# Kernel tuning notes

Measured on AMD Instinct MI355X. Metric: run time of the kernel, lower is better.

## Reference

```python
import jax, jax.numpy as jnp
import numpy as np

B, L, K = 256, 2048, 8
INV_SQRT2 = 0.7071067811865476


def _scalar_mul(d1, d2):
    # (a + b*w + c*w^2 + d*w^3)*(a' + ...) in Z[omega], omega = e^{i pi/4}, w^4 = -1
    a1, b1, c1, e1 = d1[..., 0], d1[..., 1], d1[..., 2], d1[..., 3]
    a2, b2, c2, e2 = d2[..., 0], d2[..., 1], d2[..., 2], d2[..., 3]
    A = a1 * a2 + b1 * e2 - c1 * c2 + e1 * b2
    Bc = a1 * b2 + b1 * a2 + c1 * e2 + e1 * c2
    C = a1 * c2 + b1 * b2 + c1 * a2 - e1 * e2
    D = a1 * e2 - b1 * c2 - c1 * b2 + e1 * a2
    return jnp.stack([A, Bc, C, D], axis=-1).astype(d1.dtype)


def setup_inputs() -> dict:
    key = jax.random.key(0)
    k1, k2, k3, k4 = jax.random.split(key, 4)
    coeffs1 = jax.random.randint(k1, (B, L, K, 4), 0, 2).astype(jnp.float32)
    coeffs2 = jax.random.randint(k2, (B, L, K, 4), 0, 2).astype(jnp.float32)
    power1 = jax.random.randint(k3, (B, L, K), 0, 2, dtype=jnp.int32)
    power2 = jax.random.randint(k4, (B, L, K), 0, 2, dtype=jnp.int32)
    return {"coeffs1": coeffs1, "coeffs2": coeffs2, "power1": power1, "power2": power2}


def reference(coeffs1, coeffs2, power1, power2):
    # __mul__: elementwise ring multiply, powers add
    z = _scalar_mul(coeffs1, coeffs2)          # [B,L,K,4]
    zp = power1 + power2                        # [B,L,K]

    # reduce(): divide coeffs by 2 while all even (and nonzero), bump power
    def cond_fun(carry):
        c, _ = carry
        red = jnp.all(c % 2 == 0, axis=-1) & jnp.any(c != 0, axis=-1)
        return jnp.any(red)

    def body_fun(carry):
        c, p = carry
        red = jnp.all(c % 2 == 0, axis=-1) & jnp.any(c != 0, axis=-1)
        c = jnp.where(red[..., None], c // 2, c)
        p = jnp.where(red, p + 1, p)
        return (c, p)

    c, p = jax.lax.while_loop(cond_fun, body_fun, (z, zp))

    # prod(axis=2): associative scan of the ring multiply, take last; powers sum
    scanned = jax.lax.associative_scan(_scalar_mul, c, axis=2)
    pc = scanned[:, :, -1, :]                   # [B,L,4]
    pp = jnp.sum(p, axis=2)                     # [B,L]

    # sum(): align powers to the min over L (axis=-2 of coeffs), then sum
    minp = jnp.min(pp, axis=-1)                 # [B]
    align = (2.0 ** (pp - minp[..., None])).astype(pc.dtype)
    sc = jnp.sum(pc * align[..., None], axis=-2)  # [B,4]

    # to_complex(): c0 + c1*e^{i pi/4} + c2*i + c3*e^{-i pi/4}, scaled by 2^power
    real = sc[..., 0] + (sc[..., 1] + sc[..., 3]) * INV_SQRT2
    imag = sc[..., 2] + (sc[..., 1] - sc[..., 3]) * INV_SQRT2
    scale = (2.0 ** minp).astype(sc.dtype)
    return jnp.stack([real * scale, imag * scale], axis=-1)  # [B,2] (real, imag)
```

## Files before the change

### kernel.cpp

```cpp
#include <hip/hip_runtime.h>

constexpr int BB = 256;
constexpr int LL = 2048;
constexpr int KK = 8;
constexpr int THREADS = 1024;
constexpr int SPLIT = 2;
constexpr double INV_SQRT2 = 0.7071067811865476;


__device__ __forceinline__ void ring_mul(int& ra, int& rb, int& rc, int& rd,
                                         int A, int Bv, int C, int D) {
    const int nA = __mul24(ra, A)  + __mul24(rb, D)  - __mul24(rc, C)  + __mul24(rd, Bv);
    const int nB = __mul24(ra, Bv) + __mul24(rb, A)  + __mul24(rc, D)  + __mul24(rd, C);
    const int nC = __mul24(ra, C)  + __mul24(rb, Bv) + __mul24(rc, A)  - __mul24(rd, D);
    const int nD = __mul24(ra, D)  - __mul24(rb, C)  - __mul24(rc, Bv) + __mul24(rd, A);
    ra = nA; rb = nB; rc = nC; rd = nD;
}

__device__ __forceinline__ void process(const float4 u, const float4 v, int p,
                                        const int lane, double& accR, double& accI) {
    const int a1 = (int)u.x, b1 = (int)u.y, g1 = (int)u.z, e1 = (int)u.w;
    const int a2 = (int)v.x, b2 = (int)v.y, g2 = (int)v.z, e2 = (int)v.w;

    int A  = __mul24(a1,a2) + __mul24(b1,e2) - __mul24(g1,g2) + __mul24(e1,b2);
    int Bv = __mul24(a1,b2) + __mul24(b1,a2) + __mul24(g1,e2) + __mul24(e1,g2);
    int C  = __mul24(a1,g2) + __mul24(b1,b2) + __mul24(g1,a2) - __mul24(e1,e2);
    int D  = __mul24(a1,e2) - __mul24(b1,g2) - __mul24(g1,b2) + __mul24(e1,a2);

    const int m = A | Bv | C | D;
    const int s = (m == 0) ? 0 : __builtin_ctz(m);
    A >>= s; Bv >>= s; C >>= s; D >>= s;
    p += s;

    #pragma unroll
    for (int off = 1; off < 8; off <<= 1) {
        const int oa = __shfl_xor(A,  off, 64);
        const int ob = __shfl_xor(Bv, off, 64);
        const int oc = __shfl_xor(C,  off, 64);
        const int od = __shfl_xor(D,  off, 64);
        const int op = __shfl_xor(p,  off, 64);
        ring_mul(A, Bv, C, D, oa, ob, oc, od);
        p += op;
    }

    const unsigned long long bits = ((unsigned long long)(1023 + p)) << 52;
    const double w = ((lane & 7) == 0) ? __longlong_as_double((long long)bits) : 0.0;
    const double dA = (double)A, dB = (double)Bv, dC = (double)C, dD = (double)D;
    accR += w * (dA + (dB + dD) * INV_SQRT2);
    accI += w * (dC + (dB - dD) * INV_SQRT2);
}

__global__ __launch_bounds__(THREADS) void esa_kernel(
    const float4* __restrict__ c1,
    const float4* __restrict__ c2,
    const int*  __restrict__ p1,
    const int*  __restrict__ p2,
    float* __restrict__ out) {
    const int b    = blockIdx.x >> 1;
    const int half = blockIdx.x & 1;
    const int tid  = threadIdx.x;
    const int wave = tid >> 6;
    const int lane = tid & 63;

    constexpr int LSPAN = LL / SPLIT;
    constexpr int LPW   = 16;
    constexpr int LPB   = (THREADS / 64) * LPW;
    constexpr int ITERS = LSPAN / LPB;

    double accR = 0.0, accI = 0.0;

    for (int it = 0; it < ITERS; ++it) {
        const int lbase = half * LSPAN + it * LPB + wave * LPW;
        const long long idxA = ((long long)b * LL + lbase) * KK + lane;
        const long long idxB = idxA + 64;

        const float4 uA = c1[idxA], vA = c2[idxA];
        const float4 uB = c1[idxB], vB = c2[idxB];
        const int    pA = p1[idxA] + p2[idxA];
        const int    pB = p1[idxB] + p2[idxB];

        process(uA, vA, pA, lane, accR, accI);
        process(uB, vB, pB, lane, accR, accI);
    }

    for (int off = 32; off > 0; off >>= 1) {
        accR += __shfl_down(accR, off, 64);
        accI += __shfl_down(accI, off, 64);
    }
    __shared__ double sR[THREADS / 64], sI[THREADS / 64];
    if (lane == 0) { sR[wave] = accR; sI[wave] = accI; }
    __syncthreads();
    if (tid == 0) {
        double tR = 0.0, tI = 0.0;
        #pragma unroll
        for (int w = 0; w < THREADS / 64; ++w) { tR += sR[w]; tI += sI[w]; }
        atomicAdd(&out[b * 2 + 0], (float)tR);
        atomicAdd(&out[b * 2 + 1], (float)tI);
    }
}

extern "C" void kernel_launch(void* const* d_in, const int* in_sizes, int n_in,
                              void* d_out, int out_size, void* d_ws, size_t ws_size,
                              hipStream_t stream) {
    const float4* c1 = (const float4*)d_in[0];
    const float4* c2 = (const float4*)d_in[1];
    const int*    p1 = (const int*)d_in[2];
    const int*    p2 = (const int*)d_in[3];
    float* out = (float*)d_out;

    hipMemsetAsync(out, 0, (size_t)out_size * sizeof(float), stream);
    esa_kernel<<<BB * SPLIT, THREADS, 0, stream>>>(c1, c2, p1, p2, out);
}
```

Before: 36.97 us.

## Give each thread four K-elements to multiply serially instead of a three-level shuffle scan

Each thread now handles four consecutive K entries of one product (loaded as four float4 per input plus one int4 per power array) and multiplies them serially. Only a single xor-1 shuffle step combines the two halves of each K=8 group. The grid grows to 16 blocks per batch row with 256 threads and one pass per thread, raising parallelism and removing the loop. The cost is per-thread strided float4 loads, which coalesce less well than the old lane-contiguous layout, and more atomics per output.

```diff
diff --git a/kernel.cpp b/kernel.cpp
--- a/kernel.cpp
+++ b/kernel.cpp
@@ -3,8 +3,8 @@
 constexpr int BB = 256;
 constexpr int LL = 2048;
 constexpr int KK = 8;
-constexpr int THREADS = 1024;
-constexpr int SPLIT = 2;
+constexpr int THREADS = 256;
+constexpr int SPLIT = 16;
 constexpr double INV_SQRT2 = 0.7071067811865476;
 
 
@@ -17,71 +17,63 @@
     ra = nA; rb = nB; rc = nC; rd = nD;
 }
 
-__device__ __forceinline__ void process(const float4 u, const float4 v, int p,
-                                        const int lane, double& accR, double& accI) {
+__device__ __forceinline__ int make_z(const float4 u, const float4 v,
+                                      int& A, int& Bv, int& C, int& D) {
     const int a1 = (int)u.x, b1 = (int)u.y, g1 = (int)u.z, e1 = (int)u.w;
     const int a2 = (int)v.x, b2 = (int)v.y, g2 = (int)v.z, e2 = (int)v.w;
-
-    int A  = __mul24(a1,a2) + __mul24(b1,e2) - __mul24(g1,g2) + __mul24(e1,b2);
-    int Bv = __mul24(a1,b2) + __mul24(b1,a2) + __mul24(g1,e2) + __mul24(e1,g2);
-    int C  = __mul24(a1,g2) + __mul24(b1,b2) + __mul24(g1,a2) - __mul24(e1,e2);
-    int D  = __mul24(a1,e2) - __mul24(b1,g2) - __mul24(g1,b2) + __mul24(e1,a2);
-
+    A  = __mul24(a1,a2) + __mul24(b1,e2) - __mul24(g1,g2) + __mul24(e1,b2);
+    Bv = __mul24(a1,b2) + __mul24(b1,a2) + __mul24(g1,e2) + __mul24(e1,g2);
+    C  = __mul24(a1,g2) + __mul24(b1,b2) + __mul24(g1,a2) - __mul24(e1,e2);
+    D  = __mul24(a1,e2) - __mul24(b1,g2) - __mul24(g1,b2) + __mul24(e1,a2);
     const int m = A | Bv | C | D;
     const int s = (m == 0) ? 0 : __builtin_ctz(m);
     A >>= s; Bv >>= s; C >>= s; D >>= s;
-    p += s;
-
-    #pragma unroll
-    for (int off = 1; off < 8; off <<= 1) {
-        const int oa = __shfl_xor(A,  off, 64);
-        const int ob = __shfl_xor(Bv, off, 64);
-        const int oc = __shfl_xor(C,  off, 64);
-        const int od = __shfl_xor(D,  off, 64);
-        const int op = __shfl_xor(p,  off, 64);
-        ring_mul(A, Bv, C, D, oa, ob, oc, od);
-        p += op;
-    }
-
-    const unsigned long long bits = ((unsigned long long)(1023 + p)) << 52;
-    const double w = ((lane & 7) == 0) ? __longlong_as_double((long long)bits) : 0.0;
-    const double dA = (double)A, dB = (double)Bv, dC = (double)C, dD = (double)D;
-    accR += w * (dA + (dB + dD) * INV_SQRT2);
-    accI += w * (dC + (dB - dD) * INV_SQRT2);
+    return s;
 }
 
-__global__ __launch_bounds__(THREADS) void esa_kernel(
+__global__ __launch_bounds__(THREADS, 6) void esa_kernel(
     const float4* __restrict__ c1,
     const float4* __restrict__ c2,
-    const int*  __restrict__ p1,
-    const int*  __restrict__ p2,
+    const int4*  __restrict__ p1q,
+    const int4*  __restrict__ p2q,
     float* __restrict__ out) {
-    const int b    = blockIdx.x >> 1;
-    const int half = blockIdx.x & 1;
+    const int b    = blockIdx.x >> 4;
+    const int part = blockIdx.x & 15;
     const int tid  = threadIdx.x;
     const int wave = tid >> 6;
     const int lane = tid & 63;
 
     constexpr int LSPAN = LL / SPLIT;
-    constexpr int LPW   = 16;
-    constexpr int LPB   = (THREADS / 64) * LPW;
-    constexpr int ITERS = LSPAN / LPB;
+    const long long base_e = ((long long)b * LL + part * LSPAN + wave * 32) * KK;
+    const long long te = base_e + 4LL * lane;
 
-    double accR = 0.0, accI = 0.0;
+    const float4 u0 = c1[te], u1 = c1[te + 1], u2 = c1[te + 2], u3 = c1[te + 3];
+    const float4 v0 = c2[te], v1 = c2[te + 1], v2 = c2[te + 2], v3 = c2[te + 3];
+    const int4 P1 = p1q[base_e / 4 + lane];
+    const int4 P2 = p2q[base_e / 4 + lane];
 
-    for (int it = 0; it < ITERS; ++it) {
-        const int lbase = half * LSPAN + it * LPB + wave * LPW;
-        const long long idxA = ((long long)b * LL + lbase) * KK + lane;
-        const long long idxB = idxA + 64;
+    int ra, rb, rc, rd, zA, zB, zC, zD;
+    int pp = P1.x + P2.x + make_z(u0, v0, ra, rb, rc, rd);
+    pp += P1.y + P2.y + make_z(u1, v1, zA, zB, zC, zD);
+    ring_mul(ra, rb, rc, rd, zA, zB, zC, zD);
+    pp += P1.z + P2.z + make_z(u2, v2, zA, zB, zC, zD);
+    ring_mul(ra, rb, rc, rd, zA, zB, zC, zD);
+    pp += P1.w + P2.w + make_z(u3, v3, zA, zB, zC, zD);
+    ring_mul(ra, rb, rc, rd, zA, zB, zC, zD);
 
-        const float4 uA = c1[idxA], vA = c2[idxA];
-        const float4 uB = c1[idxB], vB = c2[idxB];
-        const int    pA = p1[idxA] + p2[idxA];
-        const int    pB = p1[idxB] + p2[idxB];
+    const int oa = __shfl_xor(ra, 1, 64);
+    const int ob = __shfl_xor(rb, 1, 64);
+    const int oc = __shfl_xor(rc, 1, 64);
+    const int od = __shfl_xor(rd, 1, 64);
+    const int op = __shfl_xor(pp, 1, 64);
+    ring_mul(ra, rb, rc, rd, oa, ob, oc, od);
+    pp += op;
 
-        process(uA, vA, pA, lane, accR, accI);
-        process(uB, vB, pB, lane, accR, accI);
-    }
+    const unsigned long long bits = ((unsigned long long)(1023 + pp)) << 52;
+    const double w = ((lane & 1) == 0) ? __longlong_as_double((long long)bits) : 0.0;
+    const double dA = (double)ra, dB = (double)rb, dC = (double)rc, dD = (double)rd;
+    double accR = w * (dA + (dB + dD) * INV_SQRT2);
+    double accI = w * (dC + (dB - dD) * INV_SQRT2);
 
     for (int off = 32; off > 0; off >>= 1) {
         accR += __shfl_down(accR, off, 64);
@@ -93,7 +85,7 @@
     if (tid == 0) {
         double tR = 0.0, tI = 0.0;
         #pragma unroll
-        for (int w = 0; w < THREADS / 64; ++w) { tR += sR[w]; tI += sI[w]; }
+        for (int w2 = 0; w2 < THREADS / 64; ++w2) { tR += sR[w2]; tI += sI[w2]; }
         atomicAdd(&out[b * 2 + 0], (float)tR);
         atomicAdd(&out[b * 2 + 1], (float)tI);
     }
@@ -104,8 +96,8 @@
                               hipStream_t stream) {
     const float4* c1 = (const float4*)d_in[0];
     const float4* c2 = (const float4*)d_in[1];
-    const int*    p1 = (const int*)d_in[2];
-    const int*    p2 = (const int*)d_in[3];
+    const int4*   p1 = (const int4*)d_in[2];
+    const int4*   p2 = (const int4*)d_in[3];
     float* out = (float*)d_out;
 
     hipMemsetAsync(out, 0, (size_t)out_size * sizeof(float), stream);
```

After: 40.36 us. 1.09x slower.
